# Optimization experiments

Measured on AMD Instinct MI355X. Metric: run time of the kernel, lower is better.

The kernel has to match this reference:

```python
import jax, jax.numpy as jnp
import numpy as np

KEY_DIM = 64  # scaling uses key_dim, NOT the full projection dim (faithful to source)


def setup_inputs() -> dict:
    key = jax.random.key(0)
    ks = jax.random.split(key, 9)
    B, S, D = 4, 4096, 512
    P = 512  # heads * key_dim = 8 * 64
    s = 0.02
    return {
        "x": jax.random.normal(ks[0], (B, S, D), jnp.float32),
        "Wq": jax.random.normal(ks[1], (D, P), jnp.float32) * s,
        "bq": jnp.zeros((P,), jnp.float32),
        "Wk": jax.random.normal(ks[2], (D, P), jnp.float32) * s,
        "bk": jnp.zeros((P,), jnp.float32),
        "Wv": jax.random.normal(ks[3], (D, P), jnp.float32) * s,
        "bv": jnp.zeros((P,), jnp.float32),
        "Wo": jax.random.normal(ks[4], (P, D), jnp.float32) * s,
        "bo": jnp.zeros((D,), jnp.float32),
    }


def reference(x, Wq, bq, Wk, bk, Wv, bv, Wo, bo):
    # Manual QKV projections over the FULL heads*key_dim dim (no head split,
    # exactly as the original layer).
    q = jnp.einsum("bsd,dp->bsp", x, Wq) + bq
    k = jnp.einsum("bsd,dp->bsp", x, Wk) + bk
    v = jnp.einsum("bsd,dp->bsp", x, Wv) + bv
    scale = 1.0 / jnp.sqrt(jnp.float32(KEY_DIM))
    scores = jnp.einsum("bsp,btp->bst", q, k) * scale  # [B,S,S]
    attn = jax.nn.softmax(scores, axis=-1)
    attended = jnp.einsum("bst,btp->bsp", attn, v)
    return jnp.einsum("bsp,pd->bsd", attended, Wo) + bo
```

## Files before the change

### kernel.cpp

```cpp
#include <hip/hip_runtime.h>
#include <hip/hip_bf16.h>

typedef __bf16 bf16x8 __attribute__((ext_vector_type(8)));
typedef float  floatx4 __attribute__((ext_vector_type(4)));

#define MFMA16(a, b, c) __builtin_amdgcn_mfma_f32_16x16x32_bf16((a), (b), (c), 0, 0, 0)

static constexpr int BATCH = 4;
static constexpr int SEQ   = 4096;
static constexpr int MTOT  = BATCH * SEQ;

__device__ __forceinline__ void gload16(const void* gsrc, void* ldst)
{
    auto* g = reinterpret_cast<const __attribute__((address_space(1))) unsigned int*>(
        reinterpret_cast<unsigned long long>(gsrc));
    auto* l = reinterpret_cast<__attribute__((address_space(3))) unsigned int*>(
        reinterpret_cast<unsigned long long>(ldst));
    __builtin_amdgcn_global_load_lds(g, l, 16, 0, 0);
}

__global__ __launch_bounds__(256) void cvt_x(
    const float* __restrict__ x, __bf16* __restrict__ xb)
{
    const size_t i = ((size_t)blockIdx.x * 256 + threadIdx.x) * 8;
    const float4 a = *reinterpret_cast<const float4*>(x + i);
    const float4 c = *reinterpret_cast<const float4*>(x + i + 4);
    bf16x8 r;
    r[0] = (__bf16)a.x; r[1] = (__bf16)a.y; r[2] = (__bf16)a.z; r[3] = (__bf16)a.w;
    r[4] = (__bf16)c.x; r[5] = (__bf16)c.y; r[6] = (__bf16)c.z; r[7] = (__bf16)c.w;
    *reinterpret_cast<bf16x8*>(xb + i) = r;
}

__global__ __launch_bounds__(256) void transpose_w(
    const float* __restrict__ W, __bf16* __restrict__ WT)
{
    __shared__ __bf16 tile[64 * 68];
    const int t   = blockIdx.x;
    const int k0  = (t >> 3) * 64;
    const int n0  = (t & 7) * 64;
    const int tid = threadIdx.x;
#pragma unroll
    for (int it = 0; it < 4; ++it) {
        const int flat = it * 1024 + tid * 4;
        const int r = flat >> 6;
        const int c = flat & 63;
        const float4 v = *reinterpret_cast<const float4*>(
            W + (size_t)(k0 + r) * 512 + n0 + c);
        tile[r * 68 + c + 0] = (__bf16)v.x;
        tile[r * 68 + c + 1] = (__bf16)v.y;
        tile[r * 68 + c + 2] = (__bf16)v.z;
        tile[r * 68 + c + 3] = (__bf16)v.w;
    }
    __syncthreads();
#pragma unroll
    for (int it = 0; it < 2; ++it) {
        const int gid = it * 256 + tid;
        const int n  = gid >> 3;
        const int k8 = (gid & 7) * 8;
        bf16x8 r8;
#pragma unroll
        for (int j = 0; j < 8; ++j) r8[j] = tile[(k8 + j) * 68 + n];
        *reinterpret_cast<bf16x8*>(WT + (size_t)(n0 + n) * 512 + k0 + k8) = r8;
    }
}

__global__ __launch_bounds__(256, 2) void qkv_gemm(
    const __bf16* __restrict__ xb,
    const __bf16* __restrict__ WqT, const float* __restrict__ bq,
    const __bf16* __restrict__ WkT, const float* __restrict__ bk,
    const __bf16* __restrict__ WvT, const float* __restrict__ bv,
    __bf16* __restrict__ qb, __bf16* __restrict__ kb, __bf16* __restrict__ vbT)
{
    __shared__ __attribute__((aligned(16))) __bf16 As[128 * 64];
    __shared__ __attribute__((aligned(16))) __bf16 Bq[64 * 64];
    __shared__ __attribute__((aligned(16))) __bf16 Bk[64 * 64];
    __shared__ __attribute__((aligned(16))) __bf16 Bv[64 * 64];
    __shared__ __attribute__((aligned(16))) __bf16 Cs[64 * 144];

    const int tid  = threadIdx.x;
    const int w    = tid >> 6;
    const int lane = tid & 63;
    const int quad = lane >> 4;
    const int l15  = lane & 15;
    const int fid  = blockIdx.x;
    const int n0   = (fid & 7) * 64;
    const int m0   = (fid >> 3) * 128;

    const int srow8 = lane >> 3;
    const int sgrp  = lane & 7;

    floatx4 aq[2][4], ak[2][4], av[2][4];
#pragma unroll
    for (int rf = 0; rf < 2; ++rf)
#pragma unroll
        for (int cf = 0; cf < 4; ++cf) {
            aq[rf][cf] = floatx4{0.f, 0.f, 0.f, 0.f};
            ak[rf][cf] = floatx4{0.f, 0.f, 0.f, 0.f};
            av[rf][cf] = floatx4{0.f, 0.f, 0.f, 0.f};
        }

    for (int k0 = 0; k0 < 512; k0 += 64) {
#pragma unroll
        for (int i = 0; i < 4; ++i) {
            const int r  = w * 32 + i * 8 + srow8;
            const int cg = (sgrp ^ (r & 7)) << 3;
            gload16(xb + (size_t)(m0 + r) * 512 + k0 + cg,
                    &As[(w * 32 + i * 8) * 64]);
        }
#pragma unroll
        for (int i = 0; i < 2; ++i) {
            const int r  = w * 16 + i * 8 + srow8;
            const int cg = (sgrp ^ (r & 7)) << 3;
            const int db = (w * 16 + i * 8) * 64;
            gload16(WqT + (size_t)(n0 + r) * 512 + k0 + cg, &Bq[db]);
            gload16(WkT + (size_t)(n0 + r) * 512 + k0 + cg, &Bk[db]);
            gload16(WvT + (size_t)(n0 + r) * 512 + k0 + cg, &Bv[db]);
        }
        __syncthreads();

#pragma unroll
        for (int kk = 0; kk < 2; ++kk) {
            bf16x8 af[2];
#pragma unroll
            for (int rf = 0; rf < 2; ++rf) {
                const int arow = w * 32 + rf * 16 + l15;
                af[rf] = *reinterpret_cast<const bf16x8*>(
                    &As[arow * 64 + (((kk * 4 + quad) ^ (arow & 7)) << 3)]);
            }
#pragma unroll
            for (int cf = 0; cf < 4; ++cf) {
                const int brow = cf * 16 + l15;
                const int off  = brow * 64 + (((kk * 4 + quad) ^ (brow & 7)) << 3);
                const bf16x8 bfq = *reinterpret_cast<const bf16x8*>(&Bq[off]);
                const bf16x8 bfk = *reinterpret_cast<const bf16x8*>(&Bk[off]);
                const bf16x8 bfv = *reinterpret_cast<const bf16x8*>(&Bv[off]);
#pragma unroll
                for (int rf = 0; rf < 2; ++rf) {
                    aq[rf][cf] = MFMA16(af[rf], bfq, aq[rf][cf]);
                    ak[rf][cf] = MFMA16(af[rf], bfk, ak[rf][cf]);
                    av[rf][cf] = MFMA16(af[rf], bfv, av[rf][cf]);
                }
            }
        }
        __syncthreads();
    }

#pragma unroll
    for (int cf = 0; cf < 4; ++cf) {
        const int col = n0 + cf * 16 + l15;
        const float bqv = bq[col], bkv = bk[col], bvv = bv[col];
#pragma unroll
        for (int rf = 0; rf < 2; ++rf) {
#pragma unroll
            for (int r = 0; r < 4; ++r) {
                const int tl  = w * 32 + rf * 16 + quad * 4 + r;
                const int row = m0 + tl;
                qb[(size_t)row * 512 + col] = (__bf16)((aq[rf][cf][r] + bqv) * 0.125f);
                kb[(size_t)row * 512 + col] = (__bf16)(ak[rf][cf][r] + bkv);
                Cs[(cf * 16 + l15) * 144 + tl] = (__bf16)(av[rf][cf][r] + bvv);
            }
        }
    }
    __syncthreads();
    {
        const int bb = m0 >> 12;
        const int tb = m0 & 4095;
        __bf16* yb = vbT + (size_t)bb * 512 * 4096;
#pragma unroll
        for (int it = 0; it < 4; ++it) {
            const int flat = it * 2048 + tid * 8;
            const int pl = flat >> 7;
            const int c  = flat & 127;
            const bf16x8 vv = *reinterpret_cast<const bf16x8*>(&Cs[pl * 144 + c]);
            *reinterpret_cast<bf16x8*>(&yb[(size_t)(n0 + pl) * 4096 + tb + c]) = vv;
        }
    }
}

__global__ __launch_bounds__(256, 2) void out_gemm(
    const __bf16* __restrict__ A, const __bf16* __restrict__ WT,
    const float* __restrict__ bias, float* __restrict__ Y)
{
    __shared__ __attribute__((aligned(16))) __bf16 As[128 * 64];
    __shared__ __attribute__((aligned(16))) __bf16 Bs[128 * 64];

    const int tid  = threadIdx.x;
    const int w    = tid >> 6;
    const int lane = tid & 63;
    const int quad = lane >> 4;
    const int l15  = lane & 15;
    const int fid  = blockIdx.x;
    const int n0   = (fid & 3) * 128;
    const int m0   = (fid >> 2) * 128;

    const int srow8 = lane >> 3;
    const int sgrp  = lane & 7;

    floatx4 acc[2][8];
#pragma unroll
    for (int rf = 0; rf < 2; ++rf)
#pragma unroll
        for (int cf = 0; cf < 8; ++cf) acc[rf][cf] = floatx4{0.f, 0.f, 0.f, 0.f};

    for (int k0 = 0; k0 < 512; k0 += 64) {
#pragma unroll
        for (int i = 0; i < 4; ++i) {
            const int r  = w * 32 + i * 8 + srow8;
            const int cg = (sgrp ^ (r & 7)) << 3;
            gload16(A  + (size_t)(m0 + r) * 512 + k0 + cg,
                    &As[(w * 32 + i * 8) * 64]);
            gload16(WT + (size_t)(n0 + r) * 512 + k0 + cg,
                    &Bs[(w * 32 + i * 8) * 64]);
        }
        __syncthreads();

#pragma unroll
        for (int kk = 0; kk < 2; ++kk) {
            bf16x8 af[2];
#pragma unroll
            for (int rf = 0; rf < 2; ++rf) {
                const int arow = w * 32 + rf * 16 + l15;
                af[rf] = *reinterpret_cast<const bf16x8*>(
                    &As[arow * 64 + (((kk * 4 + quad) ^ (arow & 7)) << 3)]);
            }
#pragma unroll
            for (int cf = 0; cf < 8; ++cf) {
                const int brow = cf * 16 + l15;
                const bf16x8 bfv = *reinterpret_cast<const bf16x8*>(
                    &Bs[brow * 64 + (((kk * 4 + quad) ^ (brow & 7)) << 3)]);
#pragma unroll
                for (int rf = 0; rf < 2; ++rf)
                    acc[rf][cf] = MFMA16(af[rf], bfv, acc[rf][cf]);
            }
        }
        __syncthreads();
    }

#pragma unroll
    for (int cf = 0; cf < 8; ++cf) {
        const int col = n0 + cf * 16 + l15;
        const float bv = bias[col];
#pragma unroll
        for (int rf = 0; rf < 2; ++rf) {
#pragma unroll
            for (int r = 0; r < 4; ++r) {
                const int row = m0 + w * 32 + rf * 16 + quad * 4 + r;
                Y[(size_t)row * 512 + col] = acc[rf][cf][r] + bv;
            }
        }
    }
}

__global__ __launch_bounds__(512, 2) void flash_attn(
    const __bf16* __restrict__ q, const __bf16* __restrict__ k,
    const __bf16* __restrict__ vT, __bf16* __restrict__ pO,
    float* __restrict__ lP)
{
    __shared__ __bf16 Kt[32 * 520];
    __shared__ __bf16 Vt[512 * 32];
    __shared__ __bf16 Pl[8 * 16 * 40];

    const int tid  = threadIdx.x;
    const int w    = tid >> 6;
    const int lane = tid & 63;
    const int quad = lane >> 4;
    const int l15  = lane & 15;

    const int fid = blockIdx.x;
    const int g   = fid & 7;
    const int hb  = g & 1;
    const int b   = g >> 1;
    const int q0  = (fid >> 3) * 128;
    const size_t boff = (size_t)b * SEQ * 512;

    bf16x8 qf[16];
    {
        const __bf16* qrow = q + boff + (size_t)(q0 + w * 16 + l15) * 512;
#pragma unroll
        for (int kk = 0; kk < 16; ++kk)
            qf[kk] = *reinterpret_cast<const bf16x8*>(qrow + kk * 32 + quad * 8);
    }

    floatx4 o[32];
#pragma unroll
    for (int i = 0; i < 32; ++i) o[i] = floatx4{0.f, 0.f, 0.f, 0.f};
    float lsum[4] = {0.f, 0.f, 0.f, 0.f};

    const __bf16* kB  = k + boff;
    const __bf16* vTb = vT + boff;
    const int tstart = hb * 2048;
    const int tend   = tstart + 2048;

    const int vprow = lane >> 2;
    const int vkoff = (((lane & 3) ^ ((lane >> 3) & 3)) << 3);

    {
        const __bf16* kbase = kB + (size_t)(tstart + w * 4) * 512 + lane * 8;
#pragma unroll
        for (int j = 0; j < 4; ++j)
            gload16(kbase + (size_t)j * 512, &Kt[(w * 4 + j) * 520]);
#pragma unroll
        for (int j = 0; j < 4; ++j) {
            const int p0 = (w * 4 + j) * 16;
            gload16(vTb + (size_t)(p0 + vprow) * 4096 + tstart + vkoff, &Vt[p0 * 32]);
        }
    }

    for (int t0 = tstart; t0 < tend; t0 += 32) {
        const int tn = (t0 + 32 < tend) ? t0 + 32 : t0;

        asm volatile("s_waitcnt vmcnt(4)" ::: "memory");
        __builtin_amdgcn_s_barrier();

        floatx4 sa0 = floatx4{0.f, 0.f, 0.f, 0.f};
        floatx4 sa1 = floatx4{0.f, 0.f, 0.f, 0.f};
        __builtin_amdgcn_s_setprio(1);
#pragma unroll
        for (int kk = 0; kk < 16; ++kk) {
            const bf16x8 kf0 = *reinterpret_cast<const bf16x8*>(
                &Kt[l15 * 520 + kk * 32 + quad * 8]);
            const bf16x8 kf1 = *reinterpret_cast<const bf16x8*>(
                &Kt[(16 + l15) * 520 + kk * 32 + quad * 8]);
            sa0 = MFMA16(qf[kk], kf0, sa0);
            sa1 = MFMA16(qf[kk], kf1, sa1);
        }
        __builtin_amdgcn_s_setprio(0);

#pragma unroll
        for (int r = 0; r < 4; ++r) {
            const float p0 = __expf(sa0[r]);
            const float p1 = __expf(sa1[r]);
            lsum[r] += p0 + p1;
            Pl[(w * 16 + quad * 4 + r) * 40 + l15]      = (__bf16)p0;
            Pl[(w * 16 + quad * 4 + r) * 40 + 16 + l15] = (__bf16)p1;
        }

        __builtin_amdgcn_s_barrier();

        {
            const __bf16* kbase = kB + (size_t)(tn + w * 4) * 512 + lane * 8;
#pragma unroll
            for (int j = 0; j < 4; ++j)
                gload16(kbase + (size_t)j * 512, &Kt[(w * 4 + j) * 520]);
        }

        asm volatile("s_waitcnt vmcnt(4)" ::: "memory");
        __builtin_amdgcn_s_barrier();

        const bf16x8 pf = *reinterpret_cast<const bf16x8*>(
            &Pl[(w * 16 + l15) * 40 + quad * 8]);
        const int vsw = ((quad ^ ((l15 >> 1) & 3)) << 3);
        __builtin_amdgcn_s_setprio(1);
#pragma unroll
        for (int pt = 0; pt < 32; ++pt) {
            const bf16x8 vf = *reinterpret_cast<const bf16x8*>(
                &Vt[(pt * 16 + l15) * 32 + vsw]);
            o[pt] = MFMA16(pf, vf, o[pt]);
        }
        __builtin_amdgcn_s_setprio(0);

        __builtin_amdgcn_s_barrier();

#pragma unroll
        for (int j = 0; j < 4; ++j) {
            const int p0 = (w * 4 + j) * 16;
            gload16(vTb + (size_t)(p0 + vprow) * 4096 + tn + vkoff, &Vt[p0 * 32]);
        }
    }
    asm volatile("s_waitcnt vmcnt(0)" ::: "memory");

#pragma unroll
    for (int r = 0; r < 4; ++r) {
#pragma unroll
        for (int off = 1; off < 16; off <<= 1)
            lsum[r] += __shfl_xor(lsum[r], off);
    }
    const int rowbase = b * SEQ + q0 + w * 16 + quad * 4;
    if (l15 == 0) {
#pragma unroll
        for (int r = 0; r < 4; ++r)
            lP[(size_t)hb * MTOT + rowbase + r] = lsum[r];
    }
    __bf16* pOh = pO + (size_t)hb * MTOT * 512;
#pragma unroll
    for (int pt = 0; pt < 32; ++pt) {
#pragma unroll
        for (int r = 0; r < 4; ++r)
            pOh[(size_t)(rowbase + r) * 512 + pt * 16 + l15] = (__bf16)o[pt][r];
    }
}

__global__ __launch_bounds__(256) void merge_attn(
    const __bf16* __restrict__ pO, const float* __restrict__ lP,
    __bf16* __restrict__ att)
{
    const int gidx = blockIdx.x * 256 + threadIdx.x;
    const int row  = gidx >> 6;
    const int c8   = (gidx & 63) * 8;
    const float li = 1.0f / (lP[row] + lP[MTOT + row]);
    const bf16x8 a = *reinterpret_cast<const bf16x8*>(&pO[(size_t)row * 512 + c8]);
    const bf16x8 bvv = *reinterpret_cast<const bf16x8*>(
        &pO[((size_t)MTOT + row) * 512 + c8]);
    bf16x8 r8;
#pragma unroll
    for (int j = 0; j < 8; ++j)
        r8[j] = (__bf16)(((float)a[j] + (float)bvv[j]) * li);
    *reinterpret_cast<bf16x8*>(&att[(size_t)row * 512 + c8]) = r8;
}

extern "C" void kernel_launch(void* const* d_in, const int* in_sizes, int n_in,
                              void* d_out, int out_size, void* d_ws, size_t ws_size,
                              hipStream_t stream)
{
    (void)in_sizes; (void)n_in; (void)out_size; (void)ws_size;

    const float* x  = (const float*)d_in[0];
    const float* Wq = (const float*)d_in[1];
    const float* bq = (const float*)d_in[2];
    const float* Wk = (const float*)d_in[3];
    const float* bk = (const float*)d_in[4];
    const float* Wv = (const float*)d_in[5];
    const float* bv = (const float*)d_in[6];
    const float* Wo = (const float*)d_in[7];
    const float* bo = (const float*)d_in[8];
    float* out = (float*)d_out;

    __bf16* qb  = (__bf16*)d_ws;
    __bf16* kb  = qb  + (size_t)MTOT * 512;
    __bf16* vbT = kb  + (size_t)MTOT * 512;
    float*  lP  = (float*)(vbT + (size_t)MTOT * 512);
    __bf16* pO  = (__bf16*)d_out;
    __bf16* ab  = qb;

    __bf16* xb  = (__bf16*)d_out;
    __bf16* WqT = xb  + (size_t)MTOT * 512;
    __bf16* WkT = WqT + 512 * 512;
    __bf16* WvT = WkT + 512 * 512;
    __bf16* WoT = kb;

    cvt_x<<<MTOT * 512 / 2048, 256, 0, stream>>>(x, xb);
    transpose_w<<<64, 256, 0, stream>>>(Wq, WqT);
    transpose_w<<<64, 256, 0, stream>>>(Wk, WkT);
    transpose_w<<<64, 256, 0, stream>>>(Wv, WvT);

    qkv_gemm<<<1024, 256, 0, stream>>>(xb, WqT, bq, WkT, bk, WvT, bv, qb, kb, vbT);

    flash_attn<<<256, 512, 0, stream>>>(qb, kb, vbT, pO, lP);

    transpose_w<<<64, 256, 0, stream>>>(Wo, WoT);
    merge_attn<<<MTOT * 64 / 256, 256, 0, stream>>>(pO, lP, ab);

    out_gemm<<<512, 256, 0, stream>>>(ab, WoT, bo, out);
}
```

Baseline: 317.9 us.

## Merge prep launches, restructure PV MFMA loop, stage attention output through LDS

Measured after the change: 308.2 us. -3.1%, faster.

```diff
diff --git a/kernel.cpp b/kernel.cpp
--- a/kernel.cpp
+++ b/kernel.cpp
@@ -19,26 +19,35 @@
     __builtin_amdgcn_global_load_lds(g, l, 16, 0, 0);
 }
 
-__global__ __launch_bounds__(256) void cvt_x(
-    const float* __restrict__ x, __bf16* __restrict__ xb)
-{
-    const size_t i = ((size_t)blockIdx.x * 256 + threadIdx.x) * 8;
-    const float4 a = *reinterpret_cast<const float4*>(x + i);
-    const float4 c = *reinterpret_cast<const float4*>(x + i + 4);
-    bf16x8 r;
-    r[0] = (__bf16)a.x; r[1] = (__bf16)a.y; r[2] = (__bf16)a.z; r[3] = (__bf16)a.w;
-    r[4] = (__bf16)c.x; r[5] = (__bf16)c.y; r[6] = (__bf16)c.z; r[7] = (__bf16)c.w;
-    *reinterpret_cast<bf16x8*>(xb + i) = r;
-}
-
-__global__ __launch_bounds__(256) void transpose_w(
-    const float* __restrict__ W, __bf16* __restrict__ WT)
+__global__ __launch_bounds__(256) void prep(
+    const float* __restrict__ x, __bf16* __restrict__ xb,
+    const float* __restrict__ Wq, const float* __restrict__ Wk,
+    const float* __restrict__ Wv,
+    __bf16* __restrict__ WqT, __bf16* __restrict__ WkT, __bf16* __restrict__ WvT)
 {
     __shared__ __bf16 tile[64 * 68];
-    const int t   = blockIdx.x;
-    const int k0  = (t >> 3) * 64;
-    const int n0  = (t & 7) * 64;
+    const int bid = blockIdx.x;
     const int tid = threadIdx.x;
+
+    if (bid < 4096) {
+        const size_t i = ((size_t)bid * 256 + tid) * 8;
+        const float4 a = *reinterpret_cast<const float4*>(x + i);
+        const float4 c = *reinterpret_cast<const float4*>(x + i + 4);
+        bf16x8 r;
+        r[0] = (__bf16)a.x; r[1] = (__bf16)a.y; r[2] = (__bf16)a.z; r[3] = (__bf16)a.w;
+        r[4] = (__bf16)c.x; r[5] = (__bf16)c.y; r[6] = (__bf16)c.z; r[7] = (__bf16)c.w;
+        *reinterpret_cast<bf16x8*>(xb + i) = r;
+        return;
+    }
+
+    const int t  = bid - 4096;
+    const int m  = t >> 6;
+    const int tl = t & 63;
+    const float* W = (m == 0) ? Wq : (m == 1) ? Wk : Wv;
+    __bf16*     WT = (m == 0) ? WqT : (m == 1) ? WkT : WvT;
+    const int k0 = (tl >> 3) * 64;
+    const int n0 = (tl & 7) * 64;
+
 #pragma unroll
     for (int it = 0; it < 4; ++it) {
         const int flat = it * 1024 + tid * 4;
@@ -256,9 +265,10 @@
     const __bf16* __restrict__ vT, __bf16* __restrict__ pO,
     float* __restrict__ lP)
 {
-    __shared__ __bf16 Kt[32 * 520];
-    __shared__ __bf16 Vt[512 * 32];
-    __shared__ __bf16 Pl[8 * 16 * 40];
+    __shared__ __attribute__((aligned(16))) __bf16 SH[38144];
+    __bf16* Kt = SH;
+    __bf16* Vt = SH + 16640;
+    __bf16* Pl = SH + 33024;
 
     const int tid  = threadIdx.x;
     const int w    = tid >> 6;
@@ -293,6 +303,7 @@
 
     const int vprow = lane >> 2;
     const int vkoff = (((lane & 3) ^ ((lane >> 3) & 3)) << 3);
+    const int vsw   = ((quad ^ ((l15 >> 1) & 3)) << 3);
 
     {
         const __bf16* kbase = kB + (size_t)(tstart + w * 4) * 512 + lane * 8;
@@ -335,6 +346,7 @@
             Pl[(w * 16 + quad * 4 + r) * 40 + 16 + l15] = (__bf16)p1;
         }
 
+        asm volatile("s_waitcnt lgkmcnt(0)" ::: "memory");
         __builtin_amdgcn_s_barrier();
 
         {
@@ -347,15 +359,20 @@
         asm volatile("s_waitcnt vmcnt(4)" ::: "memory");
         __builtin_amdgcn_s_barrier();
 
-        const bf16x8 pf = *reinterpret_cast<const bf16x8*>(
-            &Pl[(w * 16 + l15) * 40 + quad * 8]);
-        const int vsw = ((quad ^ ((l15 >> 1) & 3)) << 3);
+        bf16x8 vfr[4];
+#pragma unroll
+        for (int pb = 0; pb < 4; ++pb)
+            vfr[pb] = *reinterpret_cast<const bf16x8*>(
+                &Vt[((w * 4 + pb) * 16 + l15) * 32 + vsw]);
+
         __builtin_amdgcn_s_setprio(1);
 #pragma unroll
-        for (int pt = 0; pt < 32; ++pt) {
-            const bf16x8 vf = *reinterpret_cast<const bf16x8*>(
-                &Vt[(pt * 16 + l15) * 32 + vsw]);
-            o[pt] = MFMA16(pf, vf, o[pt]);
+        for (int rb = 0; rb < 8; ++rb) {
+            const bf16x8 pf = *reinterpret_cast<const bf16x8*>(
+                &Pl[(rb * 16 + l15) * 40 + quad * 8]);
+#pragma unroll
+            for (int pb = 0; pb < 4; ++pb)
+                o[pb * 8 + rb] = MFMA16(vfr[pb], pf, o[pb * 8 + rb]);
         }
         __builtin_amdgcn_s_setprio(0);
 
@@ -375,26 +392,83 @@
         for (int off = 1; off < 16; off <<= 1)
             lsum[r] += __shfl_xor(lsum[r], off);
     }
-    const int rowbase = b * SEQ + q0 + w * 16 + quad * 4;
+    const int lrowbase = b * SEQ + q0 + w * 16 + quad * 4;
     if (l15 == 0) {
 #pragma unroll
         for (int r = 0; r < 4; ++r)
-            lP[(size_t)hb * MTOT + rowbase + r] = lsum[r];
-    }
+            lP[(size_t)hb * MTOT + lrowbase + r] = lsum[r];
+    }
+
+    __bf16* Ot = SH;
     __bf16* pOh = pO + (size_t)hb * MTOT * 512;
-#pragma unroll
-    for (int pt = 0; pt < 32; ++pt) {
-#pragma unroll
-        for (int r = 0; r < 4; ++r)
-            pOh[(size_t)(rowbase + r) * 512 + pt * 16 + l15] = (__bf16)o[pt][r];
-    }
-}
-
-__global__ __launch_bounds__(256) void merge_attn(
+    const int prowbase = b * SEQ + q0;
+#pragma unroll
+    for (int hh = 0; hh < 2; ++hh) {
+        __builtin_amdgcn_s_barrier();
+#pragma unroll
+        for (int rb2 = 0; rb2 < 4; ++rb2) {
+            const int rb = hh * 4 + rb2;
+#pragma unroll
+            for (int pb = 0; pb < 4; ++pb) {
+#pragma unroll
+                for (int r = 0; r < 4; ++r)
+                    Ot[(rb2 * 16 + l15) * 520 + (w * 4 + pb) * 16 + quad * 4 + r] =
+                        (__bf16)o[pb * 8 + rb][r];
+            }
+        }
+        asm volatile("s_waitcnt lgkmcnt(0)" ::: "memory");
+        __builtin_amdgcn_s_barrier();
+#pragma unroll
+        for (int it = 0; it < 8; ++it) {
+            const int id  = it * 512 + tid;
+            const int row = id >> 6;
+            const int c8  = (id & 63) * 8;
+            *reinterpret_cast<bf16x8*>(
+                pOh + (size_t)(prowbase + hh * 64 + row) * 512 + c8) =
+                *reinterpret_cast<const bf16x8*>(&Ot[row * 520 + c8]);
+        }
+    }
+}
+
+__global__ __launch_bounds__(256) void merge_wo(
     const __bf16* __restrict__ pO, const float* __restrict__ lP,
-    __bf16* __restrict__ att)
-{
-    const int gidx = blockIdx.x * 256 + threadIdx.x;
+    __bf16* __restrict__ att,
+    const float* __restrict__ Wo, __bf16* __restrict__ WoT)
+{
+    __shared__ __bf16 tile[64 * 68];
+    const int bid = blockIdx.x;
+    const int tid = threadIdx.x;
+
+    if (bid < 64) {
+        const int k0 = (bid >> 3) * 64;
+        const int n0 = (bid & 7) * 64;
+#pragma unroll
+        for (int it = 0; it < 4; ++it) {
+            const int flat = it * 1024 + tid * 4;
+            const int r = flat >> 6;
+            const int c = flat & 63;
+            const float4 v = *reinterpret_cast<const float4*>(
+                Wo + (size_t)(k0 + r) * 512 + n0 + c);
+            tile[r * 68 + c + 0] = (__bf16)v.x;
+            tile[r * 68 + c + 1] = (__bf16)v.y;
+            tile[r * 68 + c + 2] = (__bf16)v.z;
+            tile[r * 68 + c + 3] = (__bf16)v.w;
+        }
+        __syncthreads();
+#pragma unroll
+        for (int it = 0; it < 2; ++it) {
+            const int gid = it * 256 + tid;
+            const int n  = gid >> 3;
+            const int k8 = (gid & 7) * 8;
+            bf16x8 r8;
+#pragma unroll
+            for (int j = 0; j < 8; ++j) r8[j] = tile[(k8 + j) * 68 + n];
+            *reinterpret_cast<bf16x8*>(WoT + (size_t)(n0 + n) * 512 + k0 + k8) = r8;
+        }
+        return;
+    }
+
+    const int gidx = (bid - 64) * 256 + tid;
     const int row  = gidx >> 6;
     const int c8   = (gidx & 63) * 8;
     const float li = 1.0f / (lP[row] + lP[MTOT + row]);
@@ -438,17 +512,13 @@
     __bf16* WvT = WkT + 512 * 512;
     __bf16* WoT = kb;
 
-    cvt_x<<<MTOT * 512 / 2048, 256, 0, stream>>>(x, xb);
-    transpose_w<<<64, 256, 0, stream>>>(Wq, WqT);
-    transpose_w<<<64, 256, 0, stream>>>(Wk, WkT);
-    transpose_w<<<64, 256, 0, stream>>>(Wv, WvT);
+    prep<<<4288, 256, 0, stream>>>(x, xb, Wq, Wk, Wv, WqT, WkT, WvT);
 
     qkv_gemm<<<1024, 256, 0, stream>>>(xb, WqT, bq, WkT, bk, WvT, bv, qb, kb, vbT);
 
     flash_attn<<<256, 512, 0, stream>>>(qb, kb, vbT, pO, lP);
 
-    transpose_w<<<64, 256, 0, stream>>>(Wo, WoT);
-    merge_attn<<<MTOT * 64 / 256, 256, 0, stream>>>(pO, lP, ab);
+    merge_wo<<<4160, 256, 0, stream>>>(pO, lP, ab, Wo, WoT);
 
     out_gemm<<<512, 256, 0, stream>>>(ab, WoT, bo, out);
 }
```
